# Kernel optimization log

Hardware: AMD Instinct MI355X
Metric: run time of the kernel (lower is better)

## Reference

```python
import jax, jax.numpy as jnp
import numpy as np

EPS = 1e-5


def _extract3x3(x, stride=1):
    # channel-major patch extraction: output [B, C*9, Ho, Wo], each channel's 3x3 window contiguous
    B, C, H, W = x.shape
    xp = jnp.pad(x, ((0, 0), (0, 0), (1, 1), (1, 1)))
    Ho = (H + 2 - 3) // stride + 1
    Wo = (W + 2 - 3) // stride + 1
    pats = [xp[:, :, i:i + (Ho - 1) * stride + 1:stride, j:j + (Wo - 1) * stride + 1:stride]
            for i in range(3) for j in range(3)]
    return jnp.stack(pats, axis=2).reshape(B, C * 9, Ho, Wo)


def _amm(patches, centroids, lut, inv_temp):
    # patches: [B, D, H, W] channel-major, D = ncodebooks * subvec_len
    # centroids: [ncb, k, sub], lut: [ncb, k, out_channels]
    B, D, H, W = patches.shape
    ncb, k, sub = centroids.shape
    v = patches.reshape(B, ncb, sub, H * W).transpose(0, 3, 1, 2)  # [B, L, ncb, sub]
    # negative squared distance to each codeword (||v||^2 dropped: constant over k)
    scores = 2.0 * jnp.einsum('blcs,cks->blck', v, centroids) - jnp.sum(centroids * centroids, -1)[None, None]
    attn = jax.nn.softmax(scores * inv_temp, axis=-1)          # soft codeword assignment
    out = jnp.einsum('blck,cko->blo', attn, lut)                # LUT gather/sum over codebooks
    return out.transpose(0, 2, 1).reshape(B, -1, H, W)


def _bn(x, g, b):
    m = x.mean((0, 2, 3), keepdims=True)
    v = x.var((0, 2, 3), keepdims=True)
    return g[None, :, None, None] * (x - m) * jax.lax.rsqrt(v + EPS) + b[None, :, None, None]


def setup_inputs() -> dict:
    key = jax.random.key(0)
    ks = jax.random.split(key, 8)
    B, C, H, W = 32, 1024, 14, 14
    width, out_c, K = 256, 1024, 16
    return {
        'x': jax.random.normal(ks[0], (B, C, H, W), jnp.float32),
        'c1_centroids': jax.random.normal(ks[1], (C // 4, K, 4), jnp.float32),
        'c1_lut': jax.random.normal(ks[2], (C // 4, K, width), jnp.float32) * 0.05,
        'c1_invt': jnp.ones((), jnp.float32),
        'c2_centroids': jax.random.normal(ks[3], (width, K, 9), jnp.float32),
        'c2_lut': jax.random.normal(ks[4], (width, K, width), jnp.float32) * 0.05,
        'c2_invt': jnp.ones((), jnp.float32),
        'c3_centroids': jax.random.normal(ks[5], (width // 4, K, 4), jnp.float32),
        'c3_lut': jax.random.normal(ks[6], (width // 4, K, out_c), jnp.float32) * 0.05,
        'c3_invt': jnp.ones((), jnp.float32),
        'bn1_g': jnp.ones((width,), jnp.float32), 'bn1_b': jnp.zeros((width,), jnp.float32),
        'bn2_g': jnp.ones((width,), jnp.float32), 'bn2_b': jnp.zeros((width,), jnp.float32),
        'bn3_g': jnp.ones((out_c,), jnp.float32), 'bn3_b': jnp.zeros((out_c,), jnp.float32),
    }


def reference(x, c1_centroids, c1_lut, c1_invt, c2_centroids, c2_lut, c2_invt,
              c3_centroids, c3_lut, c3_invt, bn1_g, bn1_b, bn2_g, bn2_b, bn3_g, bn3_b):
    identity = x
    out = _amm(x, c1_centroids, c1_lut, c1_invt)                 # amm_conv1x1, stride 1
    out = jax.nn.relu(_bn(out, bn1_g, bn1_b))
    out = _amm(_extract3x3(out, 1), c2_centroids, c2_lut, c2_invt)  # amm_conv3x3, stride 1, pad 1
    out = jax.nn.relu(_bn(out, bn2_g, bn2_b))
    out = _amm(out, c3_centroids, c3_lut, c3_invt)               # amm_conv1x1
    out = _bn(out, bn3_g, bn3_b)
    return jax.nn.relu(out + identity)
```

## Files before the change

kernel.cpp:

```cpp
#include <hip/hip_runtime.h>
#include <hip/hip_bf16.h>

#define EPSV 1e-5f

typedef unsigned short u16;
typedef __attribute__((ext_vector_type(8))) short short8;
typedef __attribute__((ext_vector_type(4))) float f32x4;
typedef __hip_bfloat16 bf16;

__device__ __forceinline__ unsigned int pack2(float a, float b) {
  bf16 ha = __float2bfloat16(a), hb = __float2bfloat16(b);
  u16 ua, ub;
  __builtin_memcpy(&ua, &ha, 2);
  __builtin_memcpy(&ub, &hb, 2);
  return (unsigned int)ua | ((unsigned int)ub << 16);
}

typedef __attribute__((address_space(1))) const void gvoid_t;
typedef __attribute__((address_space(3))) void lvoid_t;
__device__ __forceinline__ void gload16(const void* g, void* l) {
  __builtin_amdgcn_global_load_lds((gvoid_t*)g, (lvoid_t*)l, 16, 0, 0);
}


__global__ __launch_bounds__(256) void lutTall_kernel(
    const float* __restrict__ s1, bf16* __restrict__ d1,
    const float* __restrict__ s2, bf16* __restrict__ d2,
    const float* __restrict__ s3, bf16* __restrict__ d3)
{
  __shared__ float t[64][65];
  const int which = blockIdx.x >> 8, bid = blockIdx.x & 255;
  const float* in = (which == 0) ? s1 : (which == 1) ? s2 : s3;
  bf16* out = (which == 0) ? d1 : (which == 1) ? d2 : d3;
  const int K = (which == 2) ? 1024 : 4096;
  const int N = (which == 2) ? 1024 : 256;
  const int kt = K >> 6;
  const int bk = bid & (kt - 1), bn = bid / kt;
  const int k0 = bk * 64, n0 = bn * 64;
  for (int idx = threadIdx.x; idx < 4096; idx += 256) {
    int r = idx >> 6, c = idx & 63;
    t[r][c] = in[(size_t)(k0 + r) * N + n0 + c];
  }
  __syncthreads();
  for (int idx = threadIdx.x; idx < 4096; idx += 256) {
    int r = idx >> 6, c = idx & 63;
    out[(size_t)(n0 + r) * K + k0 + c] = __float2bfloat16(t[c][r]);
  }
}

__global__ __launch_bounds__(256) void xT_kernel(const float* __restrict__ x,
                                                 float* __restrict__ xT)
{
  __shared__ float t[64 * 199];
  const int b = blockIdx.x >> 4, c0 = (blockIdx.x & 15) * 64;
  for (int idx = threadIdx.x; idx < 64 * 196; idx += 256) {
    int ci = idx / 196, p = idx - ci * 196;
    t[ci * 199 + p] = x[(size_t)(b * 1024 + c0 + ci) * 196 + p];
  }
  __syncthreads();
  for (int idx = threadIdx.x; idx < 196 * 64; idx += 256) {
    int p = idx >> 6, ci = idx & 63;
    xT[(size_t)(b * 196 + p) * 1024 + c0 + ci] = t[ci * 199 + p];
  }
}

__global__ __launch_bounds__(256) void attn1_kernel(const float* __restrict__ xT,
    const float* __restrict__ cent, const float* __restrict__ invt,
    u16* __restrict__ attn)
{
  __shared__ float vs[14 * 128];
  __shared__ float cs[32 * 68];
  const int tid = threadIdx.x;
  const int row = blockIdx.x >> 3, cg = blockIdx.x & 7;
  const int m0 = row * 14;
  for (int idx = tid; idx < 448; idx += 256) {
    int p = idx >> 5, c4 = idx & 31;
    *(float4*)&vs[p * 128 + c4 * 4] =
        *(const float4*)&xT[(size_t)(m0 + p) * 1024 + cg * 128 + c4 * 4];
  }
  for (int idx = tid; idx < 512; idx += 256) {
    int cb = idx >> 4, kk = idx & 15;
    *(float4*)&cs[cb * 68 + kk * 4] =
        *(const float4*)&cent[(size_t)(cg * 32 + cb) * 64 + kk * 4];
  }
  __syncthreads();
  const float it = invt[0];
  const int cb = tid & 31, pq = tid >> 5;
  const int np = (pq < 6) ? 2 : 1;
  float4 v[2];
  v[0] = *(const float4*)&vs[pq * 128 + cb * 4];
  if (np > 1) v[1] = *(const float4*)&vs[(8 + pq) * 128 + cb * 4];
  float s[2][16];
  #pragma unroll
  for (int k = 0; k < 16; k++) {
    const float4 c = *(const float4*)&cs[cb * 68 + k * 4];
    const float cn = c.x * c.x + c.y * c.y + c.z * c.z + c.w * c.w;
    #pragma unroll
    for (int i = 0; i < 2; i++) if (i < np) {
      float d = v[i].x * c.x + v[i].y * c.y + v[i].z * c.z + v[i].w * c.w;
      s[i][k] = it * (2.f * d - cn);
    }
  }
  #pragma unroll
  for (int i = 0; i < 2; i++) if (i < np) {
    float mx = -3e38f;
    #pragma unroll
    for (int k = 0; k < 16; k++) mx = fmaxf(mx, s[i][k]);
    float sum = 0.f;
    #pragma unroll
    for (int k = 0; k < 16; k++) { float e = __expf(s[i][k] - mx); s[i][k] = e; sum += e; }
    const float r = 1.f / sum;
    uint4 w0, w1;
    w0.x = pack2(s[i][0] * r,  s[i][1] * r);  w0.y = pack2(s[i][2] * r,  s[i][3] * r);
    w0.z = pack2(s[i][4] * r,  s[i][5] * r);  w0.w = pack2(s[i][6] * r,  s[i][7] * r);
    w1.x = pack2(s[i][8] * r,  s[i][9] * r);  w1.y = pack2(s[i][10] * r, s[i][11] * r);
    w1.z = pack2(s[i][12] * r, s[i][13] * r); w1.w = pack2(s[i][14] * r, s[i][15] * r);
    uint4* dst = (uint4*)(attn + (size_t)(m0 + i * 8 + pq) * 4096 + (cg * 32 + cb) * 16);
    dst[0] = w0; dst[1] = w1;
  }
}

__global__ __launch_bounds__(256) void attn2_kernel(const float* __restrict__ out1,
    const float* __restrict__ ss, const float* __restrict__ cent,
    const float* __restrict__ invt, u16* __restrict__ attn)
{
  __shared__ float vs[4 * 16 * 32];
  __shared__ __align__(16) float cs[32 * 196];
  const int tid = threadIdx.x;
  const int rp = blockIdx.x >> 3, cg = blockIdx.x & 7;
  const int b = rp / 7, y0 = (rp % 7) * 2, m0 = rp * 28;
  for (int e = tid; e < 2048; e += 256) {
    int c = e & 31, x1 = (e >> 5) & 15, dyy = e >> 9;
    int yy = y0 + dyy - 1, xx = x1 - 1;
    float v = 0.f;
    int ch = cg * 32 + c;
    if (yy >= 0 && yy < 14 && xx >= 0 && xx < 14) {
      float val = out1[(size_t)((b * 14 + yy) * 14 + xx) * 256 + ch];
      v = fmaxf(val * ss[ch] + ss[256 + ch], 0.f);
    }
    vs[e] = v;
  }
  for (int idx = tid; idx < 1152; idx += 256) {
    int cb = idx / 36, f4i = idx - cb * 36;
    float4 w = *(const float4*)&cent[(size_t)(cg * 32 + cb) * 144 + f4i * 4];
    int j0 = f4i * 4;
    #pragma unroll
    for (int t = 0; t < 4; t++) {
      int j = j0 + t, k = j / 9, jj = j - k * 9;
      cs[cb * 196 + k * 12 + jj] = ((const float*)&w)[t];
    }
  }
  __syncthreads();
  const float it = invt[0];
  const int cb = tid & 31, pq = tid >> 5;
  const int np = (pq < 4) ? 4 : 3;
  float v[4][9];
  #pragma unroll
  for (int i = 0; i < 4; i++) if (i < np) {
    const int p = i * 8 + pq;
    const int r = p / 14, xc = p - r * 14;
    #pragma unroll
    for (int dy = 0; dy < 3; dy++)
      #pragma unroll
      for (int dx = 0; dx < 3; dx++)
        v[i][dy * 3 + dx] = vs[((r + dy) * 16 + xc + dx) * 32 + cb];
  }
  float s[4][16];
  #pragma unroll
  for (int k = 0; k < 16; k++) {
    const float* ck = &cs[cb * 196 + k * 12];
    const float4 ca = *(const float4*)ck;
    const float4 cbv = *(const float4*)(ck + 4);
    const float c8 = ck[8];
    float c9[9] = {ca.x, ca.y, ca.z, ca.w, cbv.x, cbv.y, cbv.z, cbv.w, c8};
    float cn = 0.f;
    #pragma unroll
    for (int j = 0; j < 9; j++) cn = fmaf(c9[j], c9[j], cn);
    #pragma unroll
    for (int i = 0; i < 4; i++) if (i < np) {
      float d = 0.f;
      #pragma unroll
      for (int j = 0; j < 9; j++) d = fmaf(c9[j], v[i][j], d);
      s[i][k] = it * (2.f * d - cn);
    }
  }
  #pragma unroll
  for (int i = 0; i < 4; i++) if (i < np) {
    float mx = -3e38f;
    #pragma unroll
    for (int k = 0; k < 16; k++) mx = fmaxf(mx, s[i][k]);
    float sum = 0.f;
    #pragma unroll
    for (int k = 0; k < 16; k++) { float e = __expf(s[i][k] - mx); s[i][k] = e; sum += e; }
    const float r = 1.f / sum;
    uint4 w0, w1;
    w0.x = pack2(s[i][0] * r,  s[i][1] * r);  w0.y = pack2(s[i][2] * r,  s[i][3] * r);
    w0.z = pack2(s[i][4] * r,  s[i][5] * r);  w0.w = pack2(s[i][6] * r,  s[i][7] * r);
    w1.x = pack2(s[i][8] * r,  s[i][9] * r);  w1.y = pack2(s[i][10] * r, s[i][11] * r);
    w1.z = pack2(s[i][12] * r, s[i][13] * r); w1.w = pack2(s[i][14] * r, s[i][15] * r);
    uint4* dst = (uint4*)(attn + (size_t)(m0 + i * 8 + pq) * 4096 + (cg * 32 + cb) * 16);
    dst[0] = w0; dst[1] = w1;
  }
}

__global__ __launch_bounds__(256) void attn3_kernel(const float* __restrict__ out2,
    const float* __restrict__ ss, const float* __restrict__ cent,
    const float* __restrict__ invt, bf16* __restrict__ attn)
{
  const int t = threadIdx.x;
  const int cb = t & 63, ml = t >> 6;
  const int m0 = blockIdx.x * 16;
  const float it = invt[0];
  float4 cv[16]; float cn[16];
  const float4* cc = (const float4*)(cent + cb * 64);
  #pragma unroll
  for (int k = 0; k < 16; k++) {
    cv[k] = cc[k];
    cn[k] = cv[k].x * cv[k].x + cv[k].y * cv[k].y + cv[k].z * cv[k].z + cv[k].w * cv[k].w;
  }
  const float4 scv = *(const float4*)(ss + cb * 4);
  const float4 shv = *(const float4*)(ss + 256 + cb * 4);
  for (int g = 0; g < 4; g++) {
    const int m = m0 + g * 4 + ml;
    float4 xv = *(const float4*)(out2 + (size_t)m * 256 + cb * 4);
    float4 v;
    v.x = fmaxf(xv.x * scv.x + shv.x, 0.f);
    v.y = fmaxf(xv.y * scv.y + shv.y, 0.f);
    v.z = fmaxf(xv.z * scv.z + shv.z, 0.f);
    v.w = fmaxf(xv.w * scv.w + shv.w, 0.f);
    float s[16], mx = -3e38f;
    #pragma unroll
    for (int k = 0; k < 16; k++) {
      float d = v.x * cv[k].x + v.y * cv[k].y + v.z * cv[k].z + v.w * cv[k].w;
      s[k] = it * (2.f * d - cn[k]);
      mx = fmaxf(mx, s[k]);
    }
    float sum = 0.f;
    #pragma unroll
    for (int k = 0; k < 16; k++) { float e = __expf(s[k] - mx); s[k] = e; sum += e; }
    float r = 1.f / sum;
    #pragma unroll
    for (int k = 0; k < 16; k++)
      attn[(size_t)m * 1024 + cb * 16 + k] = __float2bfloat16(s[k] * r);
  }
}

template<int KDIM, int NT, int KSLICES>
__global__ __launch_bounds__(256) void gemm128_kernel(const u16* __restrict__ A,
    const u16* __restrict__ Bt, float* __restrict__ C, size_t cstride)
{
  constexpr int NDIM = NT * 128;
  constexpr int KS = KDIM / KSLICES;
  __shared__ __align__(16) u16 Asm[128 * 64];
  __shared__ __align__(16) u16 Bsm[128 * 64];
  const int tid = threadIdx.x;
  const int nt = blockIdx.x % NT;
  const int mt = (blockIdx.x / NT) % 49;
  const int sl = blockIdx.x / (NT * 49);
  const int kbeg = sl * KS, kend = kbeg + KS;
  const int m0 = mt * 128, n0 = nt * 128;
  const int lane = tid & 63, wid = tid >> 6;
  const int wm = wid >> 1, wn = wid & 1;

  const int lr = lane >> 3, js = lane & 7;

  f32x4 acc[4][4];
  #pragma unroll
  for (int i = 0; i < 4; i++)
    #pragma unroll
    for (int j = 0; j < 4; j++) acc[i][j] = (f32x4){0.f, 0.f, 0.f, 0.f};

  const u16* Abase = A + (size_t)m0 * KDIM;
  const u16* Bbase = Bt + (size_t)n0 * KDIM;

  for (int kb = kbeg; kb < kend; kb += 64) {
    #pragma unroll
    for (int c = 0; c < 4; c++) {
      const int rbase8 = (wid * 4 + c) * 8;
      const int rr = rbase8 + lr;
      const int cb = js ^ (lr);
      gload16(Abase + (size_t)rr * KDIM + kb + cb * 8, &Asm[rbase8 * 64]);
      gload16(Bbase + (size_t)rr * KDIM + kb + cb * 8, &Bsm[rbase8 * 64]);
    }
    __syncthreads();
    #pragma unroll
    for (int ks = 0; ks < 2; ks++) {
      short8 a[4], b[4];
      #pragma unroll
      for (int f = 0; f < 4; f++) {
        const int ra = wm * 64 + f * 16 + (lane & 15);
        const int ja = (ks * 4 + (lane >> 4)) ^ (ra & 7);
        a[f] = *(const short8*)(Asm + ra * 64 + ja * 8);
        const int rb = wn * 64 + f * 16 + (lane & 15);
        const int jb = (ks * 4 + (lane >> 4)) ^ (rb & 7);
        b[f] = *(const short8*)(Bsm + rb * 64 + jb * 8);
      }
      #pragma unroll
      for (int fm = 0; fm < 4; fm++)
        #pragma unroll
        for (int fn = 0; fn < 4; fn++)
          acc[fm][fn] = __builtin_amdgcn_mfma_f32_16x16x32_bf16(a[fm], b[fn], acc[fm][fn], 0, 0, 0);
    }
    __syncthreads();
  }

  float* __restrict__ Cs = C + (size_t)sl * cstride;
  #pragma unroll
  for (int fm = 0; fm < 4; fm++)
    #pragma unroll
    for (int fn = 0; fn < 4; fn++) {
      const int col = n0 + wn * 64 + fn * 16 + (lane & 15);
      const int rbase = m0 + wm * 64 + fm * 16 + (lane >> 4) * 4;
      #pragma unroll
      for (int r = 0; r < 4; r++)
        Cs[(size_t)(rbase + r) * NDIM + col] = acc[fm][fn][r];
    }
}

template<int CH, int NBLK, int NSUM>
__global__ __launch_bounds__(256) void bnpart_kernel(const float* __restrict__ buf,
    float* __restrict__ sum_out, float* __restrict__ part)
{
  constexpr int PC = CH / 256;
  constexpr int ROWS = 6272 / NBLK;
  constexpr size_t PSTR = 6272ull * CH;
  const int t = threadIdx.x, m0 = blockIdx.x * ROWS;
  float s[PC], s2[PC];
  #pragma unroll
  for (int j = 0; j < PC; j++) { s[j] = 0.f; s2[j] = 0.f; }
  for (int i = 0; i < ROWS; i++) {
    const size_t ro = (size_t)(m0 + i) * CH;
    #pragma unroll
    for (int j = 0; j < PC; j++) {
      float v = buf[ro + t + j * 256];
      #pragma unroll
      for (int n = 1; n < NSUM; n++) v += buf[(size_t)n * PSTR + ro + t + j * 256];
      if (NSUM > 1) sum_out[ro + t + j * 256] = v;
      s[j] += v; s2[j] = fmaf(v, v, s2[j]);
    }
  }
  #pragma unroll
  for (int j = 0; j < PC; j++) {
    part[(size_t)blockIdx.x * (2 * CH) + t + j * 256] = s[j];
    part[(size_t)blockIdx.x * (2 * CH) + CH + t + j * 256] = s2[j];
  }
}

template<int CH, int NBLK>
__global__ __launch_bounds__(256) void bnfin_kernel(const float* __restrict__ part,
    const float* __restrict__ g, const float* __restrict__ bb, float* __restrict__ ss)
{
  const int c = blockIdx.x * 256 + threadIdx.x;
  float S = 0.f, S2 = 0.f;
  for (int i = 0; i < NBLK; i++) {
    S += part[(size_t)i * (2 * CH) + c];
    S2 += part[(size_t)i * (2 * CH) + CH + c];
  }
  float mean = S * (1.f / 6272.f);
  float var = S2 * (1.f / 6272.f) - mean * mean;
  float sc = g[c] * rsqrtf(var + EPSV);
  ss[c] = sc;
  ss[CH + c] = bb[c] - mean * sc;
}

__global__ __launch_bounds__(256) void tfinal_kernel(const float* __restrict__ out3,
    const float* __restrict__ ss, const float* __restrict__ x, float* __restrict__ out)
{
  __shared__ float t[64 * 199];
  const int b = blockIdx.x >> 4, n0 = (blockIdx.x & 15) * 64;
  for (int idx = threadIdx.x; idx < 196 * 64; idx += 256) {
    int p = idx >> 6, ni = idx & 63;
    float v = out3[(size_t)(b * 196 + p) * 1024 + n0 + ni] * ss[n0 + ni] + ss[1024 + n0 + ni];
    t[ni * 199 + p] = v;
  }
  __syncthreads();
  for (int idx = threadIdx.x; idx < 64 * 196; idx += 256) {
    int ni = idx / 196, p = idx - ni * 196;
    size_t o = (size_t)(b * 1024 + n0 + ni) * 196 + p;
    out[o] = fmaxf(t[ni * 199 + p] + x[o], 0.f);
  }
}


template<int CIN, int OUT, bool APPLY_BN>
__global__ __launch_bounds__(256) void amm1x1_kernel(
    const float* __restrict__ xin, const float* __restrict__ ss,
    const float* __restrict__ cent, const float* __restrict__ lut,
    const float* __restrict__ invt, float* __restrict__ outbuf)
{
  constexpr int NCB = CIN / 4;
  constexpr int NO = OUT / 256;
  __shared__ float vsm[CIN * 14];
  __shared__ __align__(16) float attn_sm[14 * 16];
  const int tid = threadIdx.x;
  const int b = blockIdx.x / 14, y = blockIdx.x % 14;
  const int rowbase = y * 14;
  for (int e = tid; e < CIN * 14; e += 256) {
    int c = e / 14, xc = e - c * 14;
    float v = xin[(b * CIN + c) * 196 + rowbase + xc];
    if (APPLY_BN) v = fmaxf(v * ss[c] + ss[CIN + c], 0.f);
    vsm[e] = v;
  }
  __syncthreads();
  float acc[14 * NO];
  #pragma unroll
  for (int i = 0; i < 14 * NO; i++) acc[i] = 0.f;
  const float it = invt[0];
  const int p_ = tid >> 4, k_ = tid & 15;
  for (int cb = 0; cb < NCB; ++cb) {
    if (tid < 224) {
      const float* cc = cent + (cb * 16 + k_) * 4;
      float s = 0.f;
      #pragma unroll
      for (int si = 0; si < 4; si++) {
        float cv = cc[si];
        float vv = vsm[(cb * 4 + si) * 14 + p_];
        s = fmaf(cv, 2.f * vv - cv, s);
      }
      s *= it;
      float m = s;
      #pragma unroll
      for (int off = 8; off; off >>= 1) m = fmaxf(m, __shfl_xor(m, off, 16));
      float e = __expf(s - m);
      float sum = e;
      #pragma unroll
      for (int off = 8; off; off >>= 1) sum += __shfl_xor(sum, off, 16);
      attn_sm[p_ * 16 + k_] = e / sum;
    }
    __syncthreads();
    float lv[NO][16];
    #pragma unroll
    for (int j = 0; j < NO; j++)
      #pragma unroll
      for (int k = 0; k < 16; k++)
        lv[j][k] = lut[(cb * 16 + k) * OUT + j * 256 + tid];
    const float4* a4 = (const float4*)attn_sm;
    #pragma unroll
    for (int p = 0; p < 14; p++) {
      float4 q0 = a4[p*4+0], q1 = a4[p*4+1], q2 = a4[p*4+2], q3 = a4[p*4+3];
      float av[16] = {q0.x,q0.y,q0.z,q0.w, q1.x,q1.y,q1.z,q1.w,
                      q2.x,q2.y,q2.z,q2.w, q3.x,q3.y,q3.z,q3.w};
      #pragma unroll
      for (int j = 0; j < NO; j++) {
        float s = acc[p * NO + j];
        #pragma unroll
        for (int k = 0; k < 16; k++) s = fmaf(av[k], lv[j][k], s);
        acc[p * NO + j] = s;
      }
    }
    __syncthreads();
  }
  #pragma unroll
  for (int j = 0; j < NO; j++) {
    int o = j * 256 + tid;
    #pragma unroll
    for (int p = 0; p < 14; p++)
      outbuf[(b * OUT + o) * 196 + rowbase + p] = acc[p * NO + j];
  }
}

__global__ __launch_bounds__(256) void amm3x3_kernel(
    const float* __restrict__ xin, const float* __restrict__ ss,
    const float* __restrict__ cent, const float* __restrict__ lut,
    const float* __restrict__ invt, float* __restrict__ outbuf)
{
  __shared__ float vsm[256 * 3 * 16];
  __shared__ __align__(16) float attn_sm[14 * 16];
  const int tid = threadIdx.x;
  const int b = blockIdx.x / 14, y = blockIdx.x % 14;
  for (int e = tid; e < 256 * 3 * 16; e += 256) {
    int c = e / 48, rem = e - c * 48, i = rem >> 4, col = rem & 15;
    int yy = y + i - 1, xx = col - 1;
    float v = 0.f;
    if (yy >= 0 && yy < 14 && xx >= 0 && xx < 14) {
      v = xin[(b * 256 + c) * 196 + yy * 14 + xx];
      v = fmaxf(v * ss[c] + ss[256 + c], 0.f);
    }
    vsm[e] = v;
  }
  __syncthreads();
  float acc[14];
  #pragma unroll
  for (int i = 0; i < 14; i++) acc[i] = 0.f;
  const float it = invt[0];
  const int p_ = tid >> 4, k_ = tid & 15;
  for (int cb = 0; cb < 256; ++cb) {
    if (tid < 224) {
      const float* cc = cent + (cb * 16 + k_) * 9;
      float s = 0.f;
      #pragma unroll
      for (int i = 0; i < 3; i++)
        #pragma unroll
        for (int j = 0; j < 3; j++) {
          float cv = cc[i * 3 + j];
          float vv = vsm[(cb * 3 + i) * 16 + p_ + j];
          s = fmaf(cv, 2.f * vv - cv, s);
        }
      s *= it;
      float m = s;
      #pragma unroll
      for (int off = 8; off; off >>= 1) m = fmaxf(m, __shfl_xor(m, off, 16));
      float e = __expf(s - m);
      float sum = e;
      #pragma unroll
      for (int off = 8; off; off >>= 1) sum += __shfl_xor(sum, off, 16);
      attn_sm[p_ * 16 + k_] = e / sum;
    }
    __syncthreads();
    float lv[16];
    #pragma unroll
    for (int k = 0; k < 16; k++) lv[k] = lut[(cb * 16 + k) * 256 + tid];
    const float4* a4 = (const float4*)attn_sm;
    #pragma unroll
    for (int p = 0; p < 14; p++) {
      float4 q0 = a4[p*4+0], q1 = a4[p*4+1], q2 = a4[p*4+2], q3 = a4[p*4+3];
      float av[16] = {q0.x,q0.y,q0.z,q0.w, q1.x,q1.y,q1.z,q1.w,
                      q2.x,q2.y,q2.z,q2.w, q3.x,q3.y,q3.z,q3.w};
      float s = acc[p];
      #pragma unroll
      for (int k = 0; k < 16; k++) s = fmaf(av[k], lv[k], s);
      acc[p] = s;
    }
    __syncthreads();
  }
  #pragma unroll
  for (int p = 0; p < 14; p++)
    outbuf[(b * 256 + tid) * 196 + y * 14 + p] = acc[p];
}

template<int CH>
__global__ __launch_bounds__(256) void bnstats_kernel(const float* __restrict__ buf,
    const float* __restrict__ g, const float* __restrict__ bb, float* __restrict__ ss)
{
  const int c = blockIdx.x, tid = threadIdx.x;
  float s = 0.f, s2 = 0.f;
  for (int e = tid; e < 32 * 196; e += 256) {
    int bi = e / 196, l = e - bi * 196;
    float v = buf[(bi * CH + c) * 196 + l];
    s += v; s2 = fmaf(v, v, s2);
  }
  #pragma unroll
  for (int off = 32; off; off >>= 1) { s += __shfl_down(s, off); s2 += __shfl_down(s2, off); }
  __shared__ float red[8];
  int w = tid >> 6;
  if ((tid & 63) == 0) { red[w] = s; red[4 + w] = s2; }
  __syncthreads();
  if (tid == 0) {
    float S  = red[0] + red[1] + red[2] + red[3];
    float S2 = red[4] + red[5] + red[6] + red[7];
    float mean = S * (1.f / 6272.f);
    float var  = S2 * (1.f / 6272.f) - mean * mean;
    float sc = g[c] * rsqrtf(var + EPSV);
    ss[c] = sc;
    ss[CH + c] = bb[c] - mean * sc;
  }
}

__global__ __launch_bounds__(256) void final_old_kernel(float* __restrict__ out3,
    const float* __restrict__ ss, const float* __restrict__ x)
{
  const int total = 32 * 1024 * 196;
  for (int idx = blockIdx.x * 256 + threadIdx.x; idx < total; idx += gridDim.x * 256) {
    int c = (idx / 196) & 1023;
    float v = out3[idx] * ss[c] + ss[1024 + c] + x[idx];
    out3[idx] = fmaxf(v, 0.f);
  }
}


extern "C" void kernel_launch(void* const* d_in, const int* in_sizes, int n_in,
                              void* d_out, int out_size, void* d_ws, size_t ws_size,
                              hipStream_t stream) {
  const float* x   = (const float*)d_in[0];
  const float* c1c = (const float*)d_in[1];
  const float* c1l = (const float*)d_in[2];
  const float* c1t = (const float*)d_in[3];
  const float* c2c = (const float*)d_in[4];
  const float* c2l = (const float*)d_in[5];
  const float* c2t = (const float*)d_in[6];
  const float* c3c = (const float*)d_in[7];
  const float* c3l = (const float*)d_in[8];
  const float* c3t = (const float*)d_in[9];
  const float* g1  = (const float*)d_in[10];
  const float* b1  = (const float*)d_in[11];
  const float* g2  = (const float*)d_in[12];
  const float* b2  = (const float*)d_in[13];
  const float* g3  = (const float*)d_in[14];
  const float* b3  = (const float*)d_in[15];

  float* ws = (float*)d_ws;
  const size_t FAST_NEED = 24255488ull * 4ull;

  if (ws_size >= FAST_NEED) {
    u16*   attnB = (u16*)ws;
    float* xT    = ws + 12845056;
    float* out1  = xT + 6422528;
    float* out2  = out1 + 1605632;
    bf16*  lutT1 = (bf16*)(out2 + 1605632);
    bf16*  lutT2 = lutT1 + 1048576;
    bf16*  lutT3 = lutT2 + 1048576;
    float* part  = (float*)(lutT3 + 1048576);
    float* ss1   = part + 200704;
    float* ss2   = ss1 + 512;
    float* ss3   = ss2 + 512;
    float* out3  = xT;
    const size_t PART_STRIDE = 1605632;

    lutTall_kernel<<<768, 256, 0, stream>>>(c1l, lutT1, c2l, lutT2, c3l, lutT3);
    xT_kernel<<<512, 256, 0, stream>>>(x, xT);

    attn1_kernel<<<3584, 256, 0, stream>>>(xT, c1c, c1t, attnB);
    gemm128_kernel<4096, 2, 4><<<392, 256, 0, stream>>>(attnB, (const u16*)lutT1, xT, PART_STRIDE);
    bnpart_kernel<256, 196, 4><<<196, 256, 0, stream>>>(xT, out1, part);
    bnfin_kernel<256, 196><<<1, 256, 0, stream>>>(part, g1, b1, ss1);

    attn2_kernel<<<1792, 256, 0, stream>>>(out1, ss1, c2c, c2t, attnB);
    gemm128_kernel<4096, 2, 4><<<392, 256, 0, stream>>>(attnB, (const u16*)lutT2, xT, PART_STRIDE);
    bnpart_kernel<256, 196, 4><<<196, 256, 0, stream>>>(xT, out2, part);
    bnfin_kernel<256, 196><<<1, 256, 0, stream>>>(part, g2, b2, ss2);

    attn3_kernel<<<392, 256, 0, stream>>>(out2, ss2, c3c, c3t, (bf16*)attnB);
    gemm128_kernel<1024, 8, 1><<<392, 256, 0, stream>>>(attnB, (const u16*)lutT3, out3, 0);
    bnpart_kernel<1024, 98, 1><<<98, 256, 0, stream>>>(out3, nullptr, part);
    bnfin_kernel<1024, 98><<<4, 256, 0, stream>>>(part, g3, b3, ss3);

    tfinal_kernel<<<512, 256, 0, stream>>>(out3, ss3, x, (float*)d_out);
  } else {
    float* out3 = (float*)d_out;
    float* out1 = ws;
    float* out2 = out1 + 32 * 256 * 196;
    float* ss1  = out2 + 32 * 256 * 196;
    float* ss2  = ss1 + 512;
    float* ss3  = ss2 + 512;

    amm1x1_kernel<1024, 256, false><<<448, 256, 0, stream>>>(x, nullptr, c1c, c1l, c1t, out1);
    bnstats_kernel<256><<<256, 256, 0, stream>>>(out1, g1, b1, ss1);
    amm3x3_kernel<<<448, 256, 0, stream>>>(out1, ss1, c2c, c2l, c2t, out2);
    bnstats_kernel<256><<<256, 256, 0, stream>>>(out2, g2, b2, ss2);
    amm1x1_kernel<256, 1024, true><<<448, 256, 0, stream>>>(out2, ss2, c3c, c3l, c3t, out3);
    bnstats_kernel<1024><<<1024, 256, 0, stream>>>(out3, g3, b3, ss3);
    final_old_kernel<<<2048, 256, 0, stream>>>(out3, ss3, x);
  }
}
```

Before: 323.5 us.

## Fuse x transpose into attn1, halve GEMM M-tile, parallelize BN finalize

```diff
diff --git a/kernel.cpp b/kernel.cpp
--- a/kernel.cpp
+++ b/kernel.cpp
@@ -48,35 +48,20 @@
   }
 }
 
-__global__ __launch_bounds__(256) void xT_kernel(const float* __restrict__ x,
-                                                 float* __restrict__ xT)
-{
-  __shared__ float t[64 * 199];
-  const int b = blockIdx.x >> 4, c0 = (blockIdx.x & 15) * 64;
-  for (int idx = threadIdx.x; idx < 64 * 196; idx += 256) {
-    int ci = idx / 196, p = idx - ci * 196;
-    t[ci * 199 + p] = x[(size_t)(b * 1024 + c0 + ci) * 196 + p];
-  }
-  __syncthreads();
-  for (int idx = threadIdx.x; idx < 196 * 64; idx += 256) {
-    int p = idx >> 6, ci = idx & 63;
-    xT[(size_t)(b * 196 + p) * 1024 + c0 + ci] = t[ci * 199 + p];
-  }
-}
-
-__global__ __launch_bounds__(256) void attn1_kernel(const float* __restrict__ xT,
+__global__ __launch_bounds__(256) void attn1_kernel(const float* __restrict__ x,
     const float* __restrict__ cent, const float* __restrict__ invt,
     u16* __restrict__ attn)
 {
-  __shared__ float vs[14 * 128];
+  __shared__ float vs[14 * 132];
   __shared__ float cs[32 * 68];
   const int tid = threadIdx.x;
   const int row = blockIdx.x >> 3, cg = blockIdx.x & 7;
   const int m0 = row * 14;
-  for (int idx = tid; idx < 448; idx += 256) {
-    int p = idx >> 5, c4 = idx & 31;
-    *(float4*)&vs[p * 128 + c4 * 4] =
-        *(const float4*)&xT[(size_t)(m0 + p) * 1024 + cg * 128 + c4 * 4];
+  const int b = row / 14, y = row - b * 14;
+  const float* xb = x + ((size_t)b * 1024 + cg * 128) * 196 + y * 14;
+  for (int e = tid; e < 1792; e += 256) {
+    int c = e / 14, p = e - c * 14;
+    vs[p * 132 + c] = xb[(size_t)c * 196 + p];
   }
   for (int idx = tid; idx < 512; idx += 256) {
     int cb = idx >> 4, kk = idx & 15;
@@ -88,8 +73,8 @@
   const int cb = tid & 31, pq = tid >> 5;
   const int np = (pq < 6) ? 2 : 1;
   float4 v[2];
-  v[0] = *(const float4*)&vs[pq * 128 + cb * 4];
-  if (np > 1) v[1] = *(const float4*)&vs[(8 + pq) * 128 + cb * 4];
+  v[0] = *(const float4*)&vs[pq * 132 + cb * 4];
+  if (np > 1) v[1] = *(const float4*)&vs[(8 + pq) * 132 + cb * 4];
   float s[2][16];
   #pragma unroll
   for (int k = 0; k < 16; k++) {
@@ -245,28 +230,31 @@
   }
 }
 
-template<int KDIM, int NT, int KSLICES>
-__global__ __launch_bounds__(256) void gemm128_kernel(const u16* __restrict__ A,
+template<int KDIM, int NT, int KSLICES, int BM>
+__global__ __launch_bounds__(256) void gemm_kernel(const u16* __restrict__ A,
     const u16* __restrict__ Bt, float* __restrict__ C, size_t cstride)
 {
   constexpr int NDIM = NT * 128;
   constexpr int KS = KDIM / KSLICES;
-  __shared__ __align__(16) u16 Asm[128 * 64];
+  constexpr int MT = 6272 / BM;
+  constexpr int FM = BM / 32;
+  constexpr int ACALLS = BM / 32;
+  __shared__ __align__(16) u16 Asm[BM * 64];
   __shared__ __align__(16) u16 Bsm[128 * 64];
   const int tid = threadIdx.x;
   const int nt = blockIdx.x % NT;
-  const int mt = (blockIdx.x / NT) % 49;
-  const int sl = blockIdx.x / (NT * 49);
+  const int mt = (blockIdx.x / NT) % MT;
+  const int sl = blockIdx.x / (NT * MT);
   const int kbeg = sl * KS, kend = kbeg + KS;
-  const int m0 = mt * 128, n0 = nt * 128;
+  const int m0 = mt * BM, n0 = nt * 128;
   const int lane = tid & 63, wid = tid >> 6;
   const int wm = wid >> 1, wn = wid & 1;
-
   const int lr = lane >> 3, js = lane & 7;
-
-  f32x4 acc[4][4];
-  #pragma unroll
-  for (int i = 0; i < 4; i++)
+  const int cbs = js ^ lr;
+
+  f32x4 acc[FM][4];
+  #pragma unroll
+  for (int i = 0; i < FM; i++)
     #pragma unroll
     for (int j = 0; j < 4; j++) acc[i][j] = (f32x4){0.f, 0.f, 0.f, 0.f};
 
@@ -275,28 +263,33 @@
 
   for (int kb = kbeg; kb < kend; kb += 64) {
     #pragma unroll
+    for (int c = 0; c < ACALLS; c++) {
+      const int r8 = (wid * ACALLS + c) * 8;
+      gload16(Abase + (size_t)(r8 + lr) * KDIM + kb + cbs * 8, &Asm[r8 * 64]);
+    }
+    #pragma unroll
     for (int c = 0; c < 4; c++) {
-      const int rbase8 = (wid * 4 + c) * 8;
-      const int rr = rbase8 + lr;
-      const int cb = js ^ (lr);
-      gload16(Abase + (size_t)rr * KDIM + kb + cb * 8, &Asm[rbase8 * 64]);
-      gload16(Bbase + (size_t)rr * KDIM + kb + cb * 8, &Bsm[rbase8 * 64]);
+      const int r8 = (wid * 4 + c) * 8;
+      gload16(Bbase + (size_t)(r8 + lr) * KDIM + kb + cbs * 8, &Bsm[r8 * 64]);
     }
     __syncthreads();
     #pragma unroll
     for (int ks = 0; ks < 2; ks++) {
-      short8 a[4], b[4];
-      #pragma unroll
-      for (int f = 0; f < 4; f++) {
-        const int ra = wm * 64 + f * 16 + (lane & 15);
+      short8 a[FM], b[4];
+      #pragma unroll
+      for (int f = 0; f < FM; f++) {
+        const int ra = wm * (BM / 2) + f * 16 + (lane & 15);
         const int ja = (ks * 4 + (lane >> 4)) ^ (ra & 7);
         a[f] = *(const short8*)(Asm + ra * 64 + ja * 8);
+      }
+      #pragma unroll
+      for (int f = 0; f < 4; f++) {
         const int rb = wn * 64 + f * 16 + (lane & 15);
         const int jb = (ks * 4 + (lane >> 4)) ^ (rb & 7);
         b[f] = *(const short8*)(Bsm + rb * 64 + jb * 8);
       }
       #pragma unroll
-      for (int fm = 0; fm < 4; fm++)
+      for (int fm = 0; fm < FM; fm++)
         #pragma unroll
         for (int fn = 0; fn < 4; fn++)
           acc[fm][fn] = __builtin_amdgcn_mfma_f32_16x16x32_bf16(a[fm], b[fn], acc[fm][fn], 0, 0, 0);
@@ -306,11 +299,11 @@
 
   float* __restrict__ Cs = C + (size_t)sl * cstride;
   #pragma unroll
-  for (int fm = 0; fm < 4; fm++)
+  for (int fm = 0; fm < FM; fm++)
     #pragma unroll
     for (int fn = 0; fn < 4; fn++) {
       const int col = n0 + wn * 64 + fn * 16 + (lane & 15);
-      const int rbase = m0 + wm * 64 + fm * 16 + (lane >> 4) * 4;
+      const int rbase = m0 + wm * (BM / 2) + fm * 16 + (lane >> 4) * 4;
       #pragma unroll
       for (int r = 0; r < 4; r++)
         Cs[(size_t)(rbase + r) * NDIM + col] = acc[fm][fn][r];
@@ -350,17 +343,27 @@
 __global__ __launch_bounds__(256) void bnfin_kernel(const float* __restrict__ part,
     const float* __restrict__ g, const float* __restrict__ bb, float* __restrict__ ss)
 {
-  const int c = blockIdx.x * 256 + threadIdx.x;
+  __shared__ float red[2][4][64];
+  const int t = threadIdx.x;
+  const int chl = t & 63, grp = t >> 6;
+  const int c = blockIdx.x * 64 + chl;
   float S = 0.f, S2 = 0.f;
-  for (int i = 0; i < NBLK; i++) {
+  for (int i = grp; i < NBLK; i += 4) {
     S += part[(size_t)i * (2 * CH) + c];
     S2 += part[(size_t)i * (2 * CH) + CH + c];
   }
-  float mean = S * (1.f / 6272.f);
-  float var = S2 * (1.f / 6272.f) - mean * mean;
-  float sc = g[c] * rsqrtf(var + EPSV);
-  ss[c] = sc;
-  ss[CH + c] = bb[c] - mean * sc;
+  red[0][grp][chl] = S; red[1][grp][chl] = S2;
+  __syncthreads();
+  if (t < 64) {
+    float Sf  = red[0][0][t] + red[0][1][t] + red[0][2][t] + red[0][3][t];
+    float S2f = red[1][0][t] + red[1][1][t] + red[1][2][t] + red[1][3][t];
+    const int ch = blockIdx.x * 64 + t;
+    float mean = Sf * (1.f / 6272.f);
+    float var = S2f * (1.f / 6272.f) - mean * mean;
+    float sc = g[ch] * rsqrtf(var + EPSV);
+    ss[ch] = sc;
+    ss[CH + ch] = bb[ch] - mean * sc;
+  }
 }
 
 __global__ __launch_bounds__(256) void tfinal_kernel(const float* __restrict__ out3,
@@ -593,8 +596,8 @@
 
   if (ws_size >= FAST_NEED) {
     u16*   attnB = (u16*)ws;
-    float* xT    = ws + 12845056;
-    float* out1  = xT + 6422528;
+    float* partC = ws + 12845056;
+    float* out1  = partC + 6422528;
     float* out2  = out1 + 1605632;
     bf16*  lutT1 = (bf16*)(out2 + 1605632);
     bf16*  lutT2 = lutT1 + 1048576;
@@ -603,26 +606,25 @@
     float* ss1   = part + 200704;
     float* ss2   = ss1 + 512;
     float* ss3   = ss2 + 512;
-    float* out3  = xT;
+    float* out3  = partC;
     const size_t PART_STRIDE = 1605632;
 
     lutTall_kernel<<<768, 256, 0, stream>>>(c1l, lutT1, c2l, lutT2, c3l, lutT3);
-    xT_kernel<<<512, 256, 0, stream>>>(x, xT);
-
-    attn1_kernel<<<3584, 256, 0, stream>>>(xT, c1c, c1t, attnB);
-    gemm128_kernel<4096, 2, 4><<<392, 256, 0, stream>>>(attnB, (const u16*)lutT1, xT, PART_STRIDE);
-    bnpart_kernel<256, 196, 4><<<196, 256, 0, stream>>>(xT, out1, part);
-    bnfin_kernel<256, 196><<<1, 256, 0, stream>>>(part, g1, b1, ss1);
+
+    attn1_kernel<<<3584, 256, 0, stream>>>(x, c1c, c1t, attnB);
+    gemm_kernel<4096, 2, 4, 64><<<784, 256, 0, stream>>>(attnB, (const u16*)lutT1, partC, PART_STRIDE);
+    bnpart_kernel<256, 196, 4><<<196, 256, 0, stream>>>(partC, out1, part);
+    bnfin_kernel<256, 196><<<4, 256, 0, stream>>>(part, g1, b1, ss1);
 
     attn2_kernel<<<1792, 256, 0, stream>>>(out1, ss1, c2c, c2t, attnB);
-    gemm128_kernel<4096, 2, 4><<<392, 256, 0, stream>>>(attnB, (const u16*)lutT2, xT, PART_STRIDE);
-    bnpart_kernel<256, 196, 4><<<196, 256, 0, stream>>>(xT, out2, part);
-    bnfin_kernel<256, 196><<<1, 256, 0, stream>>>(part, g2, b2, ss2);
+    gemm_kernel<4096, 2, 4, 64><<<784, 256, 0, stream>>>(attnB, (const u16*)lutT2, partC, PART_STRIDE);
+    bnpart_kernel<256, 196, 4><<<196, 256, 0, stream>>>(partC, out2, part);
+    bnfin_kernel<256, 196><<<4, 256, 0, stream>>>(part, g2, b2, ss2);
 
     attn3_kernel<<<392, 256, 0, stream>>>(out2, ss2, c3c, c3t, (bf16*)attnB);
-    gemm128_kernel<1024, 8, 1><<<392, 256, 0, stream>>>(attnB, (const u16*)lutT3, out3, 0);
+    gemm_kernel<1024, 8, 1, 64><<<784, 256, 0, stream>>>(attnB, (const u16*)lutT3, out3, 0);
     bnpart_kernel<1024, 98, 1><<<98, 256, 0, stream>>>(out3, nullptr, part);
-    bnfin_kernel<1024, 98><<<4, 256, 0, stream>>>(part, g3, b3, ss3);
+    bnfin_kernel<1024, 98><<<16, 256, 0, stream>>>(part, g3, b3, ss3);
 
     tfinal_kernel<<<512, 256, 0, stream>>>(out3, ss3, x, (float*)d_out);
   } else {
```

Result: slower. 339.2 us (+4.9%).
